# Performance work log

Hardware: AMD Instinct MI355X
Metric: run time of the kernel (lower is better)

## Reference

```python
import jax, jax.numpy as jnp
import numpy as np

INPUT_SIZE = 1024
HIDDEN_SIZE = 1024


def setup_inputs() -> dict:
    key = jax.random.key(0)
    kq, kc, k1, k2, k3 = jax.random.split(key, 5)
    B, LQ, LC = 8, 1024, 2048
    q = jax.random.normal(kq, (B, LQ, INPUT_SIZE), dtype=jnp.float32)
    c = jax.random.normal(kc, (B, LC, INPUT_SIZE), dtype=jnp.float32)
    s = 1.0 / np.sqrt(INPUT_SIZE)
    wq = jax.random.normal(k1, (INPUT_SIZE, HIDDEN_SIZE), dtype=jnp.float32) * s
    wk = jax.random.normal(k2, (INPUT_SIZE, HIDDEN_SIZE), dtype=jnp.float32) * s
    wv = jax.random.normal(k3, (INPUT_SIZE, HIDDEN_SIZE), dtype=jnp.float32) * s
    return {"q": q, "c": c, "wq": wq, "wk": wk, "wv": wv}


def reference(q, c, wq, wk, wv):
    # Q from context c, K/V from question q (faithful to original arg wiring)
    Q = jnp.einsum('bld,dh->blh', c, wq)   # [B, LC, H]
    K = jnp.einsum('bld,dh->blh', q, wk)   # [B, LQ, H]
    V = jnp.einsum('bld,dh->blh', q, wv)   # [B, LQ, H]
    attn = jnp.einsum('bch,bqh->bcq', Q, K)  # [B, LC, LQ] (no 1/sqrt(d) scaling, as in source)
    attn = jax.nn.softmax(attn, axis=2)
    out = jnp.einsum('bcq,bqh->bch', attn, V)  # [B, LC, H]
    return out
```

## Files before the change

kernel.cpp:

```cpp
#include <hip/hip_runtime.h>
#include <stdint.h>

typedef _Float16 half8 __attribute__((ext_vector_type(8)));
typedef __attribute__((ext_vector_type(4))) float f32x4;
typedef __attribute__((ext_vector_type(4))) unsigned short us4;

__device__ __forceinline__ unsigned short f2h(float f) {
  _Float16 h = (_Float16)f;
  return __builtin_bit_cast(unsigned short, h);
}

__device__ __forceinline__ void async_cp16(const unsigned short* g, unsigned short* l) {
  __builtin_amdgcn_global_load_lds(
      (const __attribute__((address_space(1))) void*)g,
      (__attribute__((address_space(3))) void*)l, 16, 0, 0);
}

template<int EPI>
__device__ __forceinline__ void gemm_core(
    const unsigned short* __restrict__ pA, const unsigned short* __restrict__ pB,
    void* __restrict__ C0, int K, int ldc, int m0, int n0,
    unsigned short* sA, unsigned short* sB)
{
  const int t = threadIdx.x;

  const int rowS = t >> 3;
  const int kcS  = (((t & 7) - rowS) & 7) * 8;
  const long aBase = (long)(m0 + rowS) * K + kcS;
  const long bBase = (long)(n0 + rowS) * K + kcS;

  const int w  = t >> 6;
  const int l  = t & 63;
  const int wm = (w >> 1) * 64;
  const int wn = (w & 1) * 64;
  const int lm = l & 15;
  const int kquad = l >> 4;

  int offA[4][2], offB[4][2];
  #pragma unroll
  for (int i = 0; i < 4; ++i) {
    int r = wm + i * 16 + lm;
    #pragma unroll
    for (int kh = 0; kh < 2; ++kh)
      offA[i][kh] = r * 64 + ((kh * 4 + kquad + r) & 7) * 8;
  }
  #pragma unroll
  for (int j = 0; j < 4; ++j) {
    int r = wn + j * 16 + lm;
    #pragma unroll
    for (int kh = 0; kh < 2; ++kh)
      offB[j][kh] = r * 64 + ((kh * 4 + kquad + r) & 7) * 8;
  }

  f32x4 acc[4][4];
  #pragma unroll
  for (int i = 0; i < 4; ++i)
    #pragma unroll
    for (int j = 0; j < 4; ++j)
      acc[i][j] = (f32x4){0.f, 0.f, 0.f, 0.f};

  for (int k0 = 0; k0 < K; k0 += 64) {
    #pragma unroll
    for (int ci = 0; ci < 4; ++ci) {
      async_cp16(pA + aBase + (long)ci * 32 * K + k0, &sA[(ci * 256 + t) * 8]);
      async_cp16(pB + bBase + (long)ci * 32 * K + k0, &sB[(ci * 256 + t) * 8]);
    }
    __syncthreads();

    #pragma unroll
    for (int kh = 0; kh < 2; ++kh) {
      half8 bf[4];
      #pragma unroll
      for (int j = 0; j < 4; ++j)
        bf[j] = *(const half8*)&sB[offB[j][kh]];
      #pragma unroll
      for (int i = 0; i < 4; ++i) {
        half8 af = *(const half8*)&sA[offA[i][kh]];
        #pragma unroll
        for (int j = 0; j < 4; ++j)
          acc[i][j] = __builtin_amdgcn_mfma_f32_16x16x32_f16(af, bf[j], acc[i][j], 0, 0, 0);
      }
    }
    __syncthreads();
  }

  const int cr = wm + (l >> 4) * 4;
  const int cc = wn + lm;
  if (EPI == 0) {
    float* C = (float*)C0;
    #pragma unroll
    for (int i = 0; i < 4; ++i)
      #pragma unroll
      for (int j = 0; j < 4; ++j)
        #pragma unroll
        for (int r = 0; r < 4; ++r)
          C[(long)(m0 + cr + i * 16 + r) * ldc + (n0 + cc + j * 16)] = acc[i][j][r];
  } else {
    unsigned short* C = (unsigned short*)C0;
    #pragma unroll
    for (int i = 0; i < 4; ++i)
      #pragma unroll
      for (int j = 0; j < 4; ++j)
        #pragma unroll
        for (int r = 0; r < 4; ++r)
          C[(long)(m0 + cr + i * 16 + r) * ldc + (n0 + cc + j * 16)] = f2h(acc[i][j][r]);
  }
}

template<int EPI>
__global__ __launch_bounds__(256, 2)
void gemm_bt(const unsigned short* __restrict__ A, const unsigned short* __restrict__ B,
             void* __restrict__ C0,
             int K, int ldc, long aZ, long bZ, long cZ)
{
  __shared__ unsigned short sA[128 * 64];
  __shared__ unsigned short sB[128 * 64];
  const long z = blockIdx.z;
  gemm_core<EPI>(A + z * aZ, B + z * bZ,
                 (EPI == 0) ? (void*)((float*)C0 + z * cZ)
                            : (void*)((unsigned short*)C0 + z * cZ),
                 K, ldc, blockIdx.x * 128, blockIdx.y * 128, sA, sB);
}

__global__ __launch_bounds__(256, 2)
void proj_all(const unsigned short* __restrict__ ch, const unsigned short* __restrict__ qh,
              const unsigned short* __restrict__ wT,
              unsigned short* __restrict__ Qf, unsigned short* __restrict__ Kf,
              unsigned short* __restrict__ Vt)
{
  __shared__ unsigned short sA[128 * 64];
  __shared__ unsigned short sB[128 * 64];
  const int bid = blockIdx.x;
  const long qBatch = 1024l * 1024;

  const unsigned short* pA;
  const unsigned short* pB;
  unsigned short* C;
  int m0, n0;
  if (bid < 1024) {
    pA = ch; pB = wT; C = Qf;
    m0 = (bid & 127) * 128; n0 = (bid >> 7) * 128;
  } else if (bid < 1536) {
    int i = bid - 1024;
    pA = qh; pB = wT + (1l << 20); C = Kf;
    m0 = (i & 63) * 128; n0 = (i >> 6) * 128;
  } else {
    int i = bid - 1536;
    long z = i >> 6;
    pA = wT + (2l << 20); pB = qh + z * qBatch; C = Vt + z * qBatch;
    m0 = (i & 7) * 128; n0 = ((i >> 3) & 7) * 128;
  }
  gemm_core<1>(pA, pB, C, 1024, 1024, m0, n0, sA, sB);
}

__global__ __launch_bounds__(256)
void prep_all(const float* __restrict__ q, const float* __restrict__ c,
              const float* __restrict__ wq, const float* __restrict__ wk,
              const float* __restrict__ wv,
              unsigned short* __restrict__ qh, unsigned short* __restrict__ ch,
              unsigned short* __restrict__ wT)
{
  __shared__ float tile[32][33];
  const int bid = blockIdx.x;
  const int t = threadIdx.x;

  if (bid < 24576) {
    const float* x;
    unsigned short* y;
    long blk;
    if (bid < 16384) { x = c; y = ch; blk = bid; }
    else             { x = q; y = qh; blk = bid - 16384; }
    long i = (blk * 256 + t) * 4;
    float4 v = *(const float4*)(x + i);
    *(us4*)(y + i) = (us4){f2h(v.x), f2h(v.y), f2h(v.z), f2h(v.w)};
  } else {
    int i = bid - 24576;
    const int d0 = (i & 31) * 32, h0 = ((i >> 5) & 31) * 32, id = i >> 10;
    const float* W = (id == 0) ? wq : ((id == 1) ? wk : wv);
    unsigned short* WT = wT + (long)id * (1 << 20);
    #pragma unroll
    for (int p = 0; p < 4; ++p) {
      int dl = p * 8 + (t >> 5), hl = t & 31;
      tile[dl][hl] = W[(long)(d0 + dl) * 1024 + h0 + hl];
    }
    __syncthreads();
    #pragma unroll
    for (int p = 0; p < 4; ++p) {
      int hr = p * 8 + (t >> 5), dc = t & 31;
      WT[(long)(h0 + hr) * 1024 + d0 + dc] = f2h(tile[dc][hr]);
    }
  }
}

__global__ __launch_bounds__(256)
void softmax_rows(const float* __restrict__ S, unsigned short* __restrict__ P)
{
  const long row = blockIdx.x;
  const int t = threadIdx.x;
  float4 v = *(const float4*)(S + row * 1024 + t * 4);
  float m = fmaxf(fmaxf(v.x, v.y), fmaxf(v.z, v.w));
  #pragma unroll
  for (int off = 32; off > 0; off >>= 1) m = fmaxf(m, __shfl_down(m, off));
  __shared__ float red[4], red2[4];
  if ((t & 63) == 0) red[t >> 6] = m;
  __syncthreads();
  m = fmaxf(fmaxf(red[0], red[1]), fmaxf(red[2], red[3]));
  float e0 = __expf(v.x - m), e1 = __expf(v.y - m);
  float e2 = __expf(v.z - m), e3 = __expf(v.w - m);
  float sum = e0 + e1 + e2 + e3;
  #pragma unroll
  for (int off = 32; off > 0; off >>= 1) sum += __shfl_down(sum, off);
  if ((t & 63) == 0) red2[t >> 6] = sum;
  __syncthreads();
  float inv = 1.0f / (red2[0] + red2[1] + red2[2] + red2[3]);
  us4 o = {f2h(e0 * inv), f2h(e1 * inv), f2h(e2 * inv), f2h(e3 * inv)};
  *(us4*)(P + row * 1024 + t * 4) = o;
}

extern "C" void kernel_launch(void* const* d_in, const int* in_sizes, int n_in,
                              void* d_out, int out_size, void* d_ws, size_t ws_size,
                              hipStream_t stream)
{
  (void)in_sizes; (void)n_in; (void)out_size; (void)ws_size;
  const float* q  = (const float*)d_in[0];
  const float* c  = (const float*)d_in[1];
  const float* wq = (const float*)d_in[2];
  const float* wk = (const float*)d_in[3];
  const float* wv = (const float*)d_in[4];
  float* out = (float*)d_out;

  const size_t MB = 1ull << 20;
  const long cBatch = 2048l * 1024;
  const long qBatch = 1024l * 1024;

  char* ws = (char*)d_ws;
  size_t off = 0;
  auto take = [&](size_t bytes) -> unsigned short* {
    unsigned short* p = (unsigned short*)(ws + off);
    off += bytes;
    return p;
  };
  unsigned short* wT = take(6 * MB);
  unsigned short* qh = take(16 * MB);
  unsigned short* ch = take(32 * MB);
  unsigned short* Kf = take(16 * MB);
  unsigned short* Vt = take(16 * MB);
  unsigned short* Qf = take(32 * MB);
  unsigned short* Pf = ch;

  prep_all<<<27648, 256, 0, stream>>>(q, c, wq, wk, wv, qh, ch, wT);
  proj_all<<<2048, 256, 0, stream>>>(ch, qh, wT, Qf, Kf, Vt);
  gemm_bt<0><<<dim3(16, 8, 8), 256, 0, stream>>>(
      Qf, Kf, out, 1024, 1024, cBatch, qBatch, cBatch);
  softmax_rows<<<16384, 256, 0, stream>>>(out, Pf);
  gemm_bt<0><<<dim3(16, 8, 8), 256, 0, stream>>>(
      Pf, Vt, out, 1024, 1024, cBatch, qBatch, cBatch);
}
```

Measured before the change: 311.8 us.

## Replace 128x128 GEMMs with 256x256 double-buffered pipelined 512-thread GEMM kernel

Rewrites the core GEMM to use 256x256 output tiles with 8 waves, a 128KB double-buffered LDS ring split into K-halves, and async global-to-LDS prefetch interleaved with MFMA quads under explicit barriers, vmcnt waits and setprio. It also remaps block IDs for XCD-aware locality. The aim is to raise arithmetic intensity and hide global load latency behind compute. The trade-off is fewer blocks (256 or 512), which risks under-filling the 256 CUs, plus high register pressure from 32 accumulators per thread.

```diff
diff --git a/kernel.cpp b/kernel.cpp
--- a/kernel.cpp
+++ b/kernel.cpp
@@ -16,141 +16,203 @@
       (__attribute__((address_space(3))) void*)l, 16, 0, 0);
 }
 
+
+#define MFMA_QUAD(IOFF) \
+  _Pragma("unroll") \
+  for (int ii = 0; ii < 4; ++ii) { \
+    _Pragma("unroll") \
+    for (int jj = 0; jj < 4; ++jj) \
+      acc[(IOFF) + ii][jj] = __builtin_amdgcn_mfma_f32_16x16x32_f16( \
+          a[ii], b[jj], acc[(IOFF) + ii][jj], 0, 0, 0); \
+  }
+
+#define KTILE(BUF, J, ST1, ST2, WAITN) { \
+   \
+  _Pragma("unroll") \
+  for (int jj = 0; jj < 4; ++jj) b[jj] = *(const half8*)&lds[(BUF)*32768 + 16384 + offB[jj]]; \
+  _Pragma("unroll") \
+  for (int ii = 0; ii < 4; ++ii) a[ii] = *(const half8*)&lds[(BUF)*32768 + offA[ii]]; \
+  if (ST1) { const unsigned short* s_ = sA + (J + 1) * 64 + 32; \
+    async_cp16(s_ + g0, lds + (1 - (BUF)) * 32768 + 8192 + d0); \
+    async_cp16(s_ + g1, lds + (1 - (BUF)) * 32768 + 8192 + d1); } \
+  __builtin_amdgcn_s_barrier(); \
+  asm volatile("s_waitcnt lgkmcnt(0)"); \
+  __builtin_amdgcn_s_setprio(1); \
+  MFMA_QUAD(0) \
+  __builtin_amdgcn_s_setprio(0); \
+  __builtin_amdgcn_s_barrier(); \
+   \
+  _Pragma("unroll") \
+  for (int ii = 0; ii < 4; ++ii) a[ii] = *(const half8*)&lds[(BUF)*32768 + offA[4 + ii]]; \
+  if (ST1) { const unsigned short* s_ = sB + (J + 1) * 64 + 32; \
+    async_cp16(s_ + g0, lds + (1 - (BUF)) * 32768 + 24576 + d0); \
+    async_cp16(s_ + g1, lds + (1 - (BUF)) * 32768 + 24576 + d1); } \
+  __builtin_amdgcn_s_barrier(); \
+  asm volatile("s_waitcnt lgkmcnt(0)"); \
+  __builtin_amdgcn_s_setprio(1); \
+  MFMA_QUAD(4) \
+  __builtin_amdgcn_s_setprio(0); \
+  __builtin_amdgcn_s_barrier(); \
+   \
+  _Pragma("unroll") \
+  for (int jj = 0; jj < 4; ++jj) b[jj] = *(const half8*)&lds[(BUF)*32768 + 24576 + offB[jj]]; \
+  _Pragma("unroll") \
+  for (int ii = 0; ii < 4; ++ii) a[ii] = *(const half8*)&lds[(BUF)*32768 + 8192 + offA[ii]]; \
+  if (ST2) { const unsigned short* s_ = sA + (J + 2) * 64; \
+    async_cp16(s_ + g0, lds + (BUF) * 32768 + d0); \
+    async_cp16(s_ + g1, lds + (BUF) * 32768 + d1); } \
+  __builtin_amdgcn_s_barrier(); \
+  asm volatile("s_waitcnt lgkmcnt(0)"); \
+  __builtin_amdgcn_s_setprio(1); \
+  MFMA_QUAD(0) \
+  __builtin_amdgcn_s_setprio(0); \
+  __builtin_amdgcn_s_barrier(); \
+   \
+  _Pragma("unroll") \
+  for (int ii = 0; ii < 4; ++ii) a[ii] = *(const half8*)&lds[(BUF)*32768 + 8192 + offA[4 + ii]]; \
+  if (ST2) { const unsigned short* s_ = sB + (J + 2) * 64; \
+    async_cp16(s_ + g0, lds + (BUF) * 32768 + 16384 + d0); \
+    async_cp16(s_ + g1, lds + (BUF) * 32768 + 16384 + d1); } \
+  if ((WAITN) == 4)      asm volatile("s_waitcnt vmcnt(4)" ::: "memory"); \
+  else if ((WAITN) == 0) asm volatile("s_waitcnt vmcnt(0)" ::: "memory"); \
+  __builtin_amdgcn_sched_barrier(0); \
+  __builtin_amdgcn_s_barrier(); \
+  asm volatile("s_waitcnt lgkmcnt(0)"); \
+  __builtin_amdgcn_s_setprio(1); \
+  MFMA_QUAD(4) \
+  __builtin_amdgcn_s_setprio(0); \
+  __builtin_amdgcn_s_barrier(); \
+}
+
 template<int EPI>
-__device__ __forceinline__ void gemm_core(
+__device__ __forceinline__ void gemm256_core(
     const unsigned short* __restrict__ pA, const unsigned short* __restrict__ pB,
-    void* __restrict__ C0, int K, int ldc, int m0, int n0,
-    unsigned short* sA, unsigned short* sB)
+    void* __restrict__ C0, int m0, int n0, unsigned short* lds)
 {
   const int t = threadIdx.x;
 
-  const int rowS = t >> 3;
-  const int kcS  = (((t & 7) - rowS) & 7) * 8;
-  const long aBase = (long)(m0 + rowS) * K + kcS;
-  const long bBase = (long)(n0 + rowS) * K + kcS;
+  const int r0 = t >> 2;
+  const int kq0 = ((t & 3) - (r0 >> 1)) & 3;
+  const int r1 = (512 + t) >> 2;
+  const int kq1 = ((t & 3) - (r1 >> 1)) & 3;
+  const long g0 = (long)r0 * 1024 + kq0 * 8;
+  const long g1 = (long)r1 * 1024 + kq1 * 8;
+  const int d0 = t * 8;
+  const int d1 = (512 + t) * 8;
+
+  const unsigned short* sA = pA + (long)m0 * 1024;
+  const unsigned short* sB = pB + (long)n0 * 1024;
 
   const int w  = t >> 6;
   const int l  = t & 63;
-  const int wm = (w >> 1) * 64;
-  const int wn = (w & 1) * 64;
+  const int wm = (w >> 2) * 128;
+  const int wn = (w & 3) * 64;
   const int lm = l & 15;
-  const int kquad = l >> 4;
-
-  int offA[4][2], offB[4][2];
-  #pragma unroll
-  for (int i = 0; i < 4; ++i) {
+  const int kq = l >> 4;
+
+  int offA[8], offB[4];
+  #pragma unroll
+  for (int i = 0; i < 8; ++i) {
     int r = wm + i * 16 + lm;
-    #pragma unroll
-    for (int kh = 0; kh < 2; ++kh)
-      offA[i][kh] = r * 64 + ((kh * 4 + kquad + r) & 7) * 8;
+    offA[i] = r * 32 + (((kq + (r >> 1)) & 3) * 8);
   }
   #pragma unroll
   for (int j = 0; j < 4; ++j) {
     int r = wn + j * 16 + lm;
-    #pragma unroll
-    for (int kh = 0; kh < 2; ++kh)
-      offB[j][kh] = r * 64 + ((kh * 4 + kquad + r) & 7) * 8;
-  }
-
-  f32x4 acc[4][4];
-  #pragma unroll
-  for (int i = 0; i < 4; ++i)
+    offB[j] = r * 32 + (((kq + (r >> 1)) & 3) * 8);
+  }
+
+  f32x4 acc[8][4];
+  #pragma unroll
+  for (int i = 0; i < 8; ++i)
     #pragma unroll
     for (int j = 0; j < 4; ++j)
       acc[i][j] = (f32x4){0.f, 0.f, 0.f, 0.f};
 
-  for (int k0 = 0; k0 < K; k0 += 64) {
-    #pragma unroll
-    for (int ci = 0; ci < 4; ++ci) {
-      async_cp16(pA + aBase + (long)ci * 32 * K + k0, &sA[(ci * 256 + t) * 8]);
-      async_cp16(pB + bBase + (long)ci * 32 * K + k0, &sB[(ci * 256 + t) * 8]);
-    }
-    __syncthreads();
-
-    #pragma unroll
-    for (int kh = 0; kh < 2; ++kh) {
-      half8 bf[4];
-      #pragma unroll
-      for (int j = 0; j < 4; ++j)
-        bf[j] = *(const half8*)&sB[offB[j][kh]];
-      #pragma unroll
-      for (int i = 0; i < 4; ++i) {
-        half8 af = *(const half8*)&sA[offA[i][kh]];
-        #pragma unroll
-        for (int j = 0; j < 4; ++j)
-          acc[i][j] = __builtin_amdgcn_mfma_f32_16x16x32_f16(af, bf[j], acc[i][j], 0, 0, 0);
-      }
-    }
-    __syncthreads();
-  }
+  half8 a[4], b[4];
+
+  async_cp16(sA + g0,      lds + 0     + d0);  async_cp16(sA + g1,      lds + 0     + d1);
+  async_cp16(sB + g0,      lds + 16384 + d0);  async_cp16(sB + g1,      lds + 16384 + d1);
+  async_cp16(sA + g0 + 32, lds + 8192  + d0);  async_cp16(sA + g1 + 32, lds + 8192  + d1);
+  async_cp16(sB + g0 + 32, lds + 24576 + d0);  async_cp16(sB + g1 + 32, lds + 24576 + d1);
+  async_cp16(sA + g0 + 64, lds + 32768 + d0);  async_cp16(sA + g1 + 64, lds + 32768 + d1);
+  async_cp16(sB + g0 + 64, lds + 49152 + d0);  async_cp16(sB + g1 + 64, lds + 49152 + d1);
+  asm volatile("s_waitcnt vmcnt(4)" ::: "memory");
+  __builtin_amdgcn_s_barrier();
+
+  for (int j2 = 0; j2 < 7; ++j2) {
+    const int j = j2 * 2;
+    KTILE(0, j,     1, 1, 4)
+    KTILE(1, j + 1, 1, 1, 4)
+  }
+  KTILE(0, 14, 1, 0, 0)
+  KTILE(1, 15, 0, 0, -1)
 
   const int cr = wm + (l >> 4) * 4;
   const int cc = wn + lm;
   if (EPI == 0) {
     float* C = (float*)C0;
     #pragma unroll
-    for (int i = 0; i < 4; ++i)
+    for (int i = 0; i < 8; ++i)
       #pragma unroll
-      for (int j = 0; j < 4; ++j)
+      for (int jj = 0; jj < 4; ++jj)
         #pragma unroll
         for (int r = 0; r < 4; ++r)
-          C[(long)(m0 + cr + i * 16 + r) * ldc + (n0 + cc + j * 16)] = acc[i][j][r];
+          C[(long)(m0 + cr + i * 16 + r) * 1024 + (n0 + cc + jj * 16)] = acc[i][jj][r];
   } else {
     unsigned short* C = (unsigned short*)C0;
     #pragma unroll
-    for (int i = 0; i < 4; ++i)
+    for (int i = 0; i < 8; ++i)
       #pragma unroll
-      for (int j = 0; j < 4; ++j)
+      for (int jj = 0; jj < 4; ++jj)
         #pragma unroll
         for (int r = 0; r < 4; ++r)
-          C[(long)(m0 + cr + i * 16 + r) * ldc + (n0 + cc + j * 16)] = f2h(acc[i][j][r]);
-  }
-}
-
-template<int EPI>
-__global__ __launch_bounds__(256, 2)
-void gemm_bt(const unsigned short* __restrict__ A, const unsigned short* __restrict__ B,
-             void* __restrict__ C0,
-             int K, int ldc, long aZ, long bZ, long cZ)
-{
-  __shared__ unsigned short sA[128 * 64];
-  __shared__ unsigned short sB[128 * 64];
-  const long z = blockIdx.z;
-  gemm_core<EPI>(A + z * aZ, B + z * bZ,
-                 (EPI == 0) ? (void*)((float*)C0 + z * cZ)
-                            : (void*)((unsigned short*)C0 + z * cZ),
-                 K, ldc, blockIdx.x * 128, blockIdx.y * 128, sA, sB);
-}
-
-__global__ __launch_bounds__(256, 2)
-void proj_all(const unsigned short* __restrict__ ch, const unsigned short* __restrict__ qh,
-              const unsigned short* __restrict__ wT,
-              unsigned short* __restrict__ Qf, unsigned short* __restrict__ Kf,
-              unsigned short* __restrict__ Vt)
-{
-  __shared__ unsigned short sA[128 * 64];
-  __shared__ unsigned short sB[128 * 64];
+          C[(long)(m0 + cr + i * 16 + r) * 1024 + (n0 + cc + jj * 16)] = f2h(acc[i][jj][r]);
+  }
+}
+
+__global__ __launch_bounds__(512, 2)
+void gemm_bt256(const unsigned short* __restrict__ A, const unsigned short* __restrict__ B,
+                float* __restrict__ C, long aZ, long bZ, long cZ)
+{
+  __shared__ __align__(16) unsigned short lds[65536];
   const int bid = blockIdx.x;
+  const int lin = (bid & 7) * 32 + (bid >> 3);
+  const long z = lin >> 5;
+  const int rr = lin & 31;
+  gemm256_core<0>(A + z * aZ, B + z * bZ, (void*)(C + z * cZ),
+                  (rr >> 2) * 256, (rr & 3) * 256, lds);
+}
+
+__global__ __launch_bounds__(512, 2)
+void proj_all256(const unsigned short* __restrict__ ch, const unsigned short* __restrict__ qh,
+                 const unsigned short* __restrict__ wT,
+                 unsigned short* __restrict__ Qf, unsigned short* __restrict__ Kf,
+                 unsigned short* __restrict__ Vt)
+{
+  __shared__ __align__(16) unsigned short lds[65536];
+  const int bid = blockIdx.x;
+  const int lin = (bid & 7) * 64 + (bid >> 3);
   const long qBatch = 1024l * 1024;
 
   const unsigned short* pA;
   const unsigned short* pB;
   unsigned short* C;
   int m0, n0;
-  if (bid < 1024) {
+  if (lin < 256) {
     pA = ch; pB = wT; C = Qf;
-    m0 = (bid & 127) * 128; n0 = (bid >> 7) * 128;
-  } else if (bid < 1536) {
-    int i = bid - 1024;
+    m0 = (lin >> 2) * 256; n0 = (lin & 3) * 256;
+  } else if (lin < 384) {
+    int i = lin - 256;
     pA = qh; pB = wT + (1l << 20); C = Kf;
-    m0 = (i & 63) * 128; n0 = (i >> 6) * 128;
+    m0 = (i >> 2) * 256; n0 = (i & 3) * 256;
   } else {
-    int i = bid - 1536;
-    long z = i >> 6;
+    int i = lin - 384;
+    long z = i >> 4;
     pA = wT + (2l << 20); pB = qh + z * qBatch; C = Vt + z * qBatch;
-    m0 = (i & 7) * 128; n0 = ((i >> 3) & 7) * 128;
-  }
-  gemm_core<1>(pA, pB, C, 1024, 1024, m0, n0, sA, sB);
+    m0 = ((i >> 2) & 3) * 256; n0 = (i & 3) * 256;
+  }
+  gemm256_core<1>(pA, pB, C, m0, n0, lds);
 }
 
 __global__ __launch_bounds__(256)
@@ -249,10 +311,8 @@
   unsigned short* Pf = ch;
 
   prep_all<<<27648, 256, 0, stream>>>(q, c, wq, wk, wv, qh, ch, wT);
-  proj_all<<<2048, 256, 0, stream>>>(ch, qh, wT, Qf, Kf, Vt);
-  gemm_bt<0><<<dim3(16, 8, 8), 256, 0, stream>>>(
-      Qf, Kf, out, 1024, 1024, cBatch, qBatch, cBatch);
+  proj_all256<<<512, 512, 0, stream>>>(ch, qh, wT, Qf, Kf, Vt);
+  gemm_bt256<<<256, 512, 0, stream>>>(Qf, Kf, out, cBatch, qBatch, cBatch);
   softmax_rows<<<16384, 256, 0, stream>>>(out, Pf);
-  gemm_bt<0><<<dim3(16, 8, 8), 256, 0, stream>>>(
-      Pf, Vt, out, 1024, 1024, cBatch, qBatch, cBatch);
-}
+  gemm_bt256<<<256, 512, 0, stream>>>(Pf, Vt, out, cBatch, qBatch, cBatch);
+}
```

Result: faster. 303.5 us (-2.7%).
